# Optimization experiments

Measured on AMD Instinct MI355X. Metric: run time of the kernel, lower is better.

The kernel has to match this reference:

```python
import jax, jax.numpy as jnp
import numpy as np

N_NODES = 50000
N_EDGES = 800000
IN_CH = 16
OUT_CH = 16
HID = 32


def setup_inputs() -> dict:
    key = jax.random.key(0)
    ks = jax.random.split(key, 10)
    features = jax.random.normal(ks[0], (N_NODES, IN_CH), dtype=jnp.float32)
    coords = jax.random.normal(ks[1], (N_NODES, 3), dtype=jnp.float32)
    # edges without self-loops (avoids zero-distance edges)
    row = jax.random.randint(ks[2], (N_EDGES,), 0, N_NODES, dtype=jnp.int32)
    off = jax.random.randint(ks[3], (N_EDGES,), 1, N_NODES, dtype=jnp.int32)
    col = (row + off) % N_NODES
    edge_index = jnp.stack([row, col], axis=0)
    # params (fan-in scaled like torch defaults, roughly)
    w1 = jax.random.normal(ks[4], (1, HID), dtype=jnp.float32)
    b1 = jnp.zeros((HID,), dtype=jnp.float32)
    w2 = jax.random.normal(ks[5], (HID, HID), dtype=jnp.float32) / np.sqrt(HID)
    b2 = jnp.zeros((HID,), dtype=jnp.float32)
    wc = jax.random.normal(ks[6], (HID, IN_CH * OUT_CH), dtype=jnp.float32) / np.sqrt(HID)
    bc = jnp.zeros((IN_CH * OUT_CH,), dtype=jnp.float32)
    return {"features": features, "coords": coords, "edge_index": edge_index,
            "w1": w1, "b1": b1, "w2": w2, "b2": b2, "wc": wc, "bc": bc}


def reference(features, coords, edge_index, w1, b1, w2, b2, wc, bc):
    row, col = edge_index[0], edge_index[1]
    rel_pos = coords[row] - coords[col]                      # [E, 3]
    distances = jnp.sqrt(jnp.sum(rel_pos * rel_pos, axis=-1, keepdims=True))  # [E, 1]
    h = jax.nn.silu(distances @ w1 + b1)                     # [E, H]
    h = jax.nn.silu(h @ w2 + b2)                             # [E, H]
    coeffs = (h @ wc + bc).reshape(-1, OUT_CH, IN_CH)        # [E, out, in]
    # Faithful to torch einsum 'noi,ei->no': the edge axes of coeffs and
    # neighbor_features are DISTINCT labels, so features[col] is summed over
    # all edges, then contracted with each edge's coeff matrix.
    feat_sum = jnp.sum(features[col], axis=0)                # [in]
    messages = jnp.einsum('eoi,i->eo', coeffs, feat_sum)     # [E, out]
    out = jnp.zeros((features.shape[0], OUT_CH), dtype=features.dtype)
    out = out.at[row].add(messages)                          # scatter-add
    return out
```

## Files before the change

### kernel.cpp

```cpp
#include <hip/hip_runtime.h>
#include <hip/hip_bf16.h>

#define IN_CH 16
#define OUT_CH 16
#define HID 32
#define NSLICE 4
#define SDEG 32
#define CPAD 16
#define G_TAB 8192
#define DMAX 16.0f
#define RED_BLOCKS 64
#define TB 256

__device__ __forceinline__ float silu(float x) {
  return x * __frcp_rn(1.f + __expf(-x));
}

__global__ __launch_bounds__(256) void k_zero(int4* __restrict__ p, int n4) {
  int i = blockIdx.x * blockDim.x + threadIdx.x;
  if (i < n4) p[i] = make_int4(0, 0, 0, 0);
}

__global__ __launch_bounds__(256) void k_pass1(
    const float* __restrict__ feat, const float* __restrict__ coords,
    const int* __restrict__ row, const int* __restrict__ col, int E, int N,
    int* __restrict__ cnt_pad, float* __restrict__ bucket,
    float* __restrict__ partials) {
  int e = blockIdx.x * blockDim.x + threadIdx.x;
  int lane = threadIdx.x & 63;
  int wave = threadIdx.x >> 6;
  bool act = (e < E);

  float s[IN_CH];
#pragma unroll
  for (int i = 0; i < IN_CH; ++i) s[i] = 0.f;

  int r = 0, pos = SDEG;
  float d = 0.f;
  int slice = blockIdx.x & (NSLICE - 1);

  if (act) {
    r = row[e];
    int c = col[e];

    float rx = coords[r * 3 + 0] - coords[c * 3 + 0];
    float ry = coords[r * 3 + 1] - coords[c * 3 + 1];
    float rz = coords[r * 3 + 2] - coords[c * 3 + 2];
    d = sqrtf(rx * rx + ry * ry + rz * rz);

    pos = atomicAdd(&cnt_pad[((size_t)r * NSLICE + slice) * CPAD], 1);

    const float4* fp = reinterpret_cast<const float4*>(feat + (size_t)c * IN_CH);
    float4 a = fp[0], b = fp[1], cc = fp[2], dd = fp[3];
    s[0] = a.x;  s[1] = a.y;  s[2] = a.z;  s[3] = a.w;
    s[4] = b.x;  s[5] = b.y;  s[6] = b.z;  s[7] = b.w;
    s[8] = cc.x; s[9] = cc.y; s[10] = cc.z; s[11] = cc.w;
    s[12] = dd.x; s[13] = dd.y; s[14] = dd.z; s[15] = dd.w;
  }

  __shared__ float red[4][IN_CH];
#pragma unroll
  for (int i = 0; i < IN_CH; ++i) {
    float v = s[i];
#pragma unroll
    for (int off = 32; off > 0; off >>= 1) v += __shfl_down(v, off);
    s[i] = v;
  }
  if (lane == 0) {
#pragma unroll
    for (int i = 0; i < IN_CH; ++i) red[wave][i] = s[i];
  }
  __syncthreads();
  if (threadIdx.x < IN_CH) {
    int i = threadIdx.x;
    partials[(size_t)blockIdx.x * IN_CH + i] =
        red[0][i] + red[1][i] + red[2][i] + red[3][i];
  }

  if (act && pos < SDEG)
    bucket[((size_t)r * NSLICE + slice) * SDEG + pos] = d;
}

__global__ __launch_bounds__(256) void k_red(
    const float* __restrict__ partials, int nrows,
    const float* __restrict__ wc, const float* __restrict__ bc,
    float* __restrict__ stage2, int* __restrict__ done,
    float* __restrict__ wce, float* __restrict__ bce) {
  __shared__ float red[16][IN_CH];
  __shared__ float sfs[IN_CH];
  __shared__ int lastFlag;
  int t = threadIdx.x;
  int ch = t & 15, g = t >> 4;

  {
    int stream_id = blockIdx.x * 16 + g;
    int stride = 16 * RED_BLOCKS;
    float a = 0.f;
    for (int rr = stream_id; rr < nrows; rr += stride)
      a += partials[(size_t)rr * IN_CH + ch];
    red[g][ch] = a;
  }
  __syncthreads();
  if (t < IN_CH) {
    float s = 0.f;
#pragma unroll
    for (int g2 = 0; g2 < 16; ++g2) s += red[g2][t];
    stage2[blockIdx.x * IN_CH + t] = s;
  }
  __threadfence();
  __syncthreads();
  if (t == 0) lastFlag = (atomicAdd(done, 1) == RED_BLOCKS - 1);
  __syncthreads();
  if (!lastFlag) return;

  __threadfence();
  {
    int sg = t >> 4;
    float a = 0.f;
    for (int rr = sg; rr < RED_BLOCKS; rr += 16)
      a += stage2[rr * IN_CH + ch];
    red[sg][ch] = a;
  }
  __syncthreads();
  if (t < IN_CH) {
    float s = 0.f;
#pragma unroll
    for (int g2 = 0; g2 < 16; ++g2) s += red[g2][t];
    sfs[t] = s;
  }
  __syncthreads();

  for (int idx = t; idx < HID * OUT_CH; idx += 256) {
    int k = idx >> 4, o = idx & 15;
    float acc = 0.f;
#pragma unroll
    for (int i = 0; i < IN_CH; ++i)
      acc += wc[k * (IN_CH * OUT_CH) + o * IN_CH + i] * sfs[i];
    wce[idx] = acc;
  }
  if (t < OUT_CH) {
    float a = 0.f;
#pragma unroll
    for (int i = 0; i < IN_CH; ++i) a += bc[t * IN_CH + i] * sfs[i];
    bce[t] = a;
  }
}

__global__ __launch_bounds__(TB) void k_table(
    const float* __restrict__ w1, const float* __restrict__ b1,
    const float* __restrict__ w2, const float* __restrict__ b2,
    const float* __restrict__ wce, const float* __restrict__ bce,
    float* __restrict__ tableP) {
  __shared__ float F[TB][OUT_CH];
  int base = blockIdx.x * (TB - 1);
  int i = base + threadIdx.x;

  float m[OUT_CH];
#pragma unroll
  for (int o = 0; o < OUT_CH; ++o) m[o] = 0.f;

  if (i < G_TAB) {
    float d = (float)i * (DMAX / (float)(G_TAB - 1));

    float h1[HID];
#pragma unroll
    for (int k = 0; k < HID; ++k) h1[k] = silu(d * w1[k] + b1[k]);

    float h2[HID];
#pragma unroll
    for (int k = 0; k < HID; ++k) h2[k] = b2[k];
#pragma unroll
    for (int k = 0; k < HID; ++k) {
      float hk = h1[k];
#pragma unroll
      for (int j = 0; j < HID; ++j) h2[j] += hk * w2[k * HID + j];
    }

#pragma unroll
    for (int o = 0; o < OUT_CH; ++o) m[o] = bce[o];
#pragma unroll
    for (int k = 0; k < HID; ++k) {
      float hk = silu(h2[k]);
#pragma unroll
      for (int o = 0; o < OUT_CH; ++o) m[o] += hk * wce[k * OUT_CH + o];
    }
  }

#pragma unroll
  for (int o = 0; o < OUT_CH; ++o) F[threadIdx.x][o] = m[o];
  __syncthreads();

  const int NV4 = (TB - 1) * OUT_CH * 2 / 4;
  for (int v = threadIdx.x; v < NV4; v += TB) {
    int flat = v * 4;
    int p = flat >> 5;
    int w = flat & 31;
    int c0 = w >> 1;
    int P = base + p;
    if (P < G_TAB - 1) {
      float4 val = make_float4(F[p][c0], F[p + 1][c0],
                               F[p][c0 + 1], F[p + 1][c0 + 1]);
      *reinterpret_cast<float4*>(tableP + ((size_t)P * OUT_CH + c0) * 2) = val;
    }
  }
}

__global__ __launch_bounds__(256) void k_gather_tab(
    const int* __restrict__ cnt_pad, const float* __restrict__ bucket, int N,
    const float* __restrict__ tableP, float* __restrict__ out) {
  int wave = threadIdx.x >> 6;
  int lane = threadIdx.x & 63;
  int n = blockIdx.x * 4 + wave;
  if (n >= N) return;

  int g = lane >> 4;
  int ch = lane & 15;

  const float2* bp =
      reinterpret_cast<const float2*>(bucket + (size_t)n * (NSLICE * SDEG));
  float2 d2 = bp[lane];

  int c = 0;
  if (lane < NSLICE) c = cnt_pad[((size_t)n * NSLICE + lane) * CPAD];
  int c0 = min(__shfl(c, 0), SDEG);
  int c1 = min(__shfl(c, 1), SDEG);
  int c2 = min(__shfl(c, 2), SDEG);
  int c3 = min(__shfl(c, 3), SDEG);
  int cntG = (g == 0) ? c0 : (g == 1) ? c1 : (g == 2) ? c2 : c3;
  int jmax = max(max(c0, c1), max(c2, c3));

  const float inv = (float)(G_TAB - 1) / DMAX;
  float acc = 0.f;
  for (int j = 0; j < jmax; j += 2) {
    int half = (g * SDEG + j) >> 1;
    float da = __shfl(d2.x, half);
    float db = __shfl(d2.y, half);
    bool pa = (j < cntG), pb = (j + 1 < cntG);

    da = fminf(fmaxf(da, 0.f), DMAX);
    db = fminf(fmaxf(db, 0.f), DMAX);
    float xa = da * inv;
    int ia = min((int)xa, G_TAB - 2);
    float fa = xa - (float)ia;
    float xb = db * inv;
    int ib = min((int)xb, G_TAB - 2);
    float fb = xb - (float)ib;

    if (pa) {
      float2 F = *reinterpret_cast<const float2*>(
          tableP + ((size_t)ia * OUT_CH + ch) * 2);
      acc += F.x + fa * (F.y - F.x);
    }
    if (pb) {
      float2 F = *reinterpret_cast<const float2*>(
          tableP + ((size_t)ib * OUT_CH + ch) * 2);
      acc += F.x + fb * (F.y - F.x);
    }
  }

  acc += __shfl_xor(acc, 16);
  acc += __shfl_xor(acc, 32);
  if (lane < OUT_CH) out[(size_t)n * OUT_CH + lane] = acc;
}

__global__ __launch_bounds__(512) void k_wce_fb(
    const float* __restrict__ rows_in, int nrows,
    const float* __restrict__ wc, const float* __restrict__ bc,
    float* __restrict__ wce, float* __restrict__ bce) {
  __shared__ float seg[32][IN_CH];
  __shared__ float sfs[IN_CH];
  int t = threadIdx.x;
  {
    int ch = t & 15, sg = t >> 4;
    float a = 0.f;
    for (int rr = sg; rr < nrows; rr += 32)
      a += rows_in[(size_t)rr * IN_CH + ch];
    seg[sg][ch] = a;
  }
  __syncthreads();
  if (t < IN_CH) {
    float a = 0.f;
#pragma unroll
    for (int sg = 0; sg < 32; ++sg) a += seg[sg][t];
    sfs[t] = a;
  }
  __syncthreads();
  int k = t >> 4, o = t & 15;
  float acc = 0.f;
#pragma unroll
  for (int i = 0; i < IN_CH; ++i)
    acc += wc[k * (IN_CH * OUT_CH) + o * IN_CH + i] * sfs[i];
  wce[t] = acc;
  if (t < OUT_CH) {
    float a = 0.f;
#pragma unroll
    for (int i = 0; i < IN_CH; ++i) a += bc[t * IN_CH + i] * sfs[i];
    bce[t] = a;
  }
}

__global__ __launch_bounds__(256) void k_hist(
    const int* __restrict__ col, int E, int* __restrict__ ccnt) {
  int e = blockIdx.x * blockDim.x + threadIdx.x;
  if (e < E) atomicAdd(&ccnt[col[e]], 1);
}

__global__ __launch_bounds__(256) void k_fs(
    const float* __restrict__ feat, const int* __restrict__ ccnt, int N,
    float* __restrict__ partials) {
  int ch = threadIdx.x & 15;
  int slot = threadIdx.x >> 4;
  int gs = blockIdx.x * 16 + slot;
  int stride = 16 * gridDim.x;
  float a = 0.f;
  for (int n = gs; n < N; n += stride)
    a += (float)ccnt[n] * feat[(size_t)n * IN_CH + ch];
  __shared__ float red[16][IN_CH];
  red[slot][ch] = a;
  __syncthreads();
  if (threadIdx.x < IN_CH) {
    int i = threadIdx.x;
    float s = 0.f;
#pragma unroll
    for (int g = 0; g < 16; ++g) s += red[g][i];
    partials[(size_t)blockIdx.x * IN_CH + i] = s;
  }
}

__global__ __launch_bounds__(256) void k_edges_atomic(
    const float* __restrict__ coords, const int* __restrict__ row,
    const int* __restrict__ col, int E,
    const float* __restrict__ w1, const float* __restrict__ b1,
    const float* __restrict__ w2, const float* __restrict__ b2,
    const float* __restrict__ wce, const float* __restrict__ bce,
    float* __restrict__ out) {
  int e = blockIdx.x * blockDim.x + threadIdx.x;
  if (e >= E) return;
  int r = row[e], c = col[e];
  float rx = coords[r * 3 + 0] - coords[c * 3 + 0];
  float ry = coords[r * 3 + 1] - coords[c * 3 + 1];
  float rz = coords[r * 3 + 2] - coords[c * 3 + 2];
  float d = sqrtf(rx * rx + ry * ry + rz * rz);
  float h1[HID];
#pragma unroll
  for (int k = 0; k < HID; ++k) h1[k] = silu(d * w1[k] + b1[k]);
  float h2[HID];
#pragma unroll
  for (int k = 0; k < HID; ++k) h2[k] = b2[k];
#pragma unroll
  for (int k = 0; k < HID; ++k) {
    float hk = h1[k];
#pragma unroll
    for (int j = 0; j < HID; ++j) h2[j] += hk * w2[k * HID + j];
  }
  float m[OUT_CH];
#pragma unroll
  for (int o = 0; o < OUT_CH; ++o) m[o] = bce[o];
#pragma unroll
  for (int k = 0; k < HID; ++k) {
    float hk = silu(h2[k]);
#pragma unroll
    for (int o = 0; o < OUT_CH; ++o) m[o] += hk * wce[k * OUT_CH + o];
  }
  float* op = out + (size_t)r * OUT_CH;
#pragma unroll
  for (int o = 0; o < OUT_CH; ++o) atomicAdd(op + o, m[o]);
}

extern "C" void kernel_launch(void* const* d_in, const int* in_sizes, int n_in,
                              void* d_out, int out_size, void* d_ws,
                              size_t ws_size, hipStream_t stream) {
  const float* features = (const float*)d_in[0];
  const float* coords   = (const float*)d_in[1];
  const int*   eidx     = (const int*)d_in[2];
  const float* w1       = (const float*)d_in[3];
  const float* b1       = (const float*)d_in[4];
  const float* w2       = (const float*)d_in[5];
  const float* b2       = (const float*)d_in[6];
  const float* wc       = (const float*)d_in[7];
  const float* bc       = (const float*)d_in[8];

  const int E = in_sizes[2] / 2;
  const int N = in_sizes[0] / IN_CH;
  const int* row = eidx;
  const int* col = eidx + E;

  float* out = (float*)d_out;
  float* ws  = (float*)d_ws;
  const int eb = (E + 255) / 256;

  size_t off = 0;
  float* wce = ws + off;      off += 512;
  float* bce = ws + off;      off += 16;
  float* stage2 = ws + off;   off += RED_BLOCKS * IN_CH;
  float* partials = ws + off; off += (size_t)eb * IN_CH;
  off = (off + 63) & ~(size_t)63;
  float* tableP = ws + off;   off += (size_t)G_TAB * OUT_CH * 2;
  off = (off + 63) & ~(size_t)63;
  int* done = (int*)(ws + off);     off += 16;
  int* cnt_pad = (int*)(ws + off);  off += (size_t)N * NSLICE * CPAD;
  float* bucket = ws + off;         off += (size_t)N * NSLICE * SDEG;
  size_t needed = off * 4;

  if (ws_size >= needed) {
    int n4 = (int)((16 + (size_t)N * NSLICE * CPAD) / 4);
    k_zero<<<(n4 + 255) / 256, 256, 0, stream>>>((int4*)done, n4);
    k_pass1<<<eb, 256, 0, stream>>>(features, coords, row, col, E, N, cnt_pad,
                                    bucket, partials);
    k_red<<<RED_BLOCKS, 256, 0, stream>>>(partials, eb, wc, bc, stage2, done,
                                          wce, bce);
    int tb_grid = (G_TAB - 1 + (TB - 1) - 1) / (TB - 1) + 1;
    k_table<<<tb_grid, TB, 0, stream>>>(w1, b1, w2, b2, wce, bce, tableP);
    int gb = (N + 3) / 4;
    k_gather_tab<<<gb, 256, 0, stream>>>(cnt_pad, bucket, N, tableP, out);
  } else {
    float* partials_fb = bce + 16;
    int*   ccnt_fb     = (int*)(partials_fb + 64 * IN_CH);
    int nz4 = (N + 3) / 4;
    k_zero<<<(nz4 + 255) / 256, 256, 0, stream>>>((int4*)ccnt_fb, nz4);
    hipMemsetAsync(out, 0, (size_t)out_size * sizeof(float), stream);
    k_hist<<<(E + 255) / 256, 256, 0, stream>>>(col, E, ccnt_fb);
    k_fs<<<64, 256, 0, stream>>>(features, ccnt_fb, N, partials_fb);
    k_wce_fb<<<1, 512, 0, stream>>>(partials_fb, 64, wc, bc, wce, bce);
    k_edges_atomic<<<(E + 255) / 256, 256, 0, stream>>>(coords, row, col, E,
                                                        w1, b1, w2, b2, wce,
                                                        bce, out);
  }
}
```

Baseline: 101.1 us.

## Compact slice counters, interleave bucket layout, make gather persistent with prefetch

Per-node slice counters are no longer padded to 16 ints each. They are packed into four contiguous ints, which shrinks the buffer that has to be zeroed every call and makes the count reads dense. The distance bucket is reordered to [node][pos][slice], so one 64-lane load covers the first 16 positions of all slices; positions beyond 16 are read from global memory. The gather kernel becomes a grid-stride persistent kernel of 1024 blocks that prefetches the next node's bucket and counts. The distance clamp to DMAX is dropped in favour of clamping only the table index, so distances above DMAX would extrapolate past the last table entry.

```diff
diff --git a/kernel.cpp b/kernel.cpp
--- a/kernel.cpp
+++ b/kernel.cpp
@@ -6,11 +6,11 @@
 #define HID 32
 #define NSLICE 4
 #define SDEG 32
-#define CPAD 16
 #define G_TAB 8192
 #define DMAX 16.0f
 #define RED_BLOCKS 64
 #define TB 256
+#define GB_BLOCKS 1024
 
 __device__ __forceinline__ float silu(float x) {
   return x * __frcp_rn(1.f + __expf(-x));
@@ -24,7 +24,7 @@
 __global__ __launch_bounds__(256) void k_pass1(
     const float* __restrict__ feat, const float* __restrict__ coords,
     const int* __restrict__ row, const int* __restrict__ col, int E, int N,
-    int* __restrict__ cnt_pad, float* __restrict__ bucket,
+    int* __restrict__ cnt4, float* __restrict__ bucket,
     float* __restrict__ partials) {
   int e = blockIdx.x * blockDim.x + threadIdx.x;
   int lane = threadIdx.x & 63;
@@ -48,7 +48,7 @@
     float rz = coords[r * 3 + 2] - coords[c * 3 + 2];
     d = sqrtf(rx * rx + ry * ry + rz * rz);
 
-    pos = atomicAdd(&cnt_pad[((size_t)r * NSLICE + slice) * CPAD], 1);
+    pos = atomicAdd(&cnt4[r * NSLICE + slice], 1);
 
     const float4* fp = reinterpret_cast<const float4*>(feat + (size_t)c * IN_CH);
     float4 a = fp[0], b = fp[1], cc = fp[2], dd = fp[3];
@@ -78,7 +78,7 @@
   }
 
   if (act && pos < SDEG)
-    bucket[((size_t)r * NSLICE + slice) * SDEG + pos] = d;
+    bucket[((size_t)r * SDEG + pos) * NSLICE + slice] = d;
 }
 
 __global__ __launch_bounds__(256) void k_red(
@@ -206,61 +206,75 @@
 }
 
 __global__ __launch_bounds__(256) void k_gather_tab(
-    const int* __restrict__ cnt_pad, const float* __restrict__ bucket, int N,
+    const int* __restrict__ cnt4, const float* __restrict__ bucket, int N,
     const float* __restrict__ tableP, float* __restrict__ out) {
   int wave = threadIdx.x >> 6;
   int lane = threadIdx.x & 63;
+  int g = lane >> 4;
+  int ch = lane & 15;
+  const int nwaves = GB_BLOCKS * 4;
+
   int n = blockIdx.x * 4 + wave;
   if (n >= N) return;
 
-  int g = lane >> 4;
-  int ch = lane & 15;
-
-  const float2* bp =
-      reinterpret_cast<const float2*>(bucket + (size_t)n * (NSLICE * SDEG));
-  float2 d2 = bp[lane];
-
-  int c = 0;
-  if (lane < NSLICE) c = cnt_pad[((size_t)n * NSLICE + lane) * CPAD];
-  int c0 = min(__shfl(c, 0), SDEG);
-  int c1 = min(__shfl(c, 1), SDEG);
-  int c2 = min(__shfl(c, 2), SDEG);
-  int c3 = min(__shfl(c, 3), SDEG);
-  int cntG = (g == 0) ? c0 : (g == 1) ? c1 : (g == 2) ? c2 : c3;
-  int jmax = max(max(c0, c1), max(c2, c3));
-
   const float inv = (float)(G_TAB - 1) / DMAX;
-  float acc = 0.f;
-  for (int j = 0; j < jmax; j += 2) {
-    int half = (g * SDEG + j) >> 1;
-    float da = __shfl(d2.x, half);
-    float db = __shfl(d2.y, half);
-    bool pa = (j < cntG), pb = (j + 1 < cntG);
-
-    da = fminf(fmaxf(da, 0.f), DMAX);
-    db = fminf(fmaxf(db, 0.f), DMAX);
-    float xa = da * inv;
-    int ia = min((int)xa, G_TAB - 2);
-    float fa = xa - (float)ia;
-    float xb = db * inv;
-    int ib = min((int)xb, G_TAB - 2);
-    float fb = xb - (float)ib;
-
-    if (pa) {
-      float2 F = *reinterpret_cast<const float2*>(
-          tableP + ((size_t)ia * OUT_CH + ch) * 2);
-      acc += F.x + fa * (F.y - F.x);
+
+  float dpre = bucket[(size_t)n * (SDEG * NSLICE) + lane];
+  int cpre = (lane < NSLICE) ? cnt4[n * NSLICE + lane] : 0;
+
+  while (true) {
+    float dcur = dpre;
+    int ccur = cpre;
+    int nn = n + nwaves;
+    if (nn < N) {
+      dpre = bucket[(size_t)nn * (SDEG * NSLICE) + lane];
+      cpre = (lane < NSLICE) ? cnt4[nn * NSLICE + lane] : 0;
     }
-    if (pb) {
-      float2 F = *reinterpret_cast<const float2*>(
-          tableP + ((size_t)ib * OUT_CH + ch) * 2);
-      acc += F.x + fb * (F.y - F.x);
+
+    int c0 = min(__shfl(ccur, 0), SDEG);
+    int c1 = min(__shfl(ccur, 1), SDEG);
+    int c2 = min(__shfl(ccur, 2), SDEG);
+    int c3 = min(__shfl(ccur, 3), SDEG);
+    int cntG = (g == 0) ? c0 : (g == 1) ? c1 : (g == 2) ? c2 : c3;
+    int jmax = max(max(c0, c1), max(c2, c3));
+
+    const float* nb = bucket + (size_t)n * (SDEG * NSLICE);
+    float acc = 0.f;
+    for (int j = 0; j < jmax; j += 2) {
+      float da = __shfl(dcur, j * NSLICE + g);
+      float db = __shfl(dcur, (j + 1) * NSLICE + g);
+      if (j >= 16) da = nb[j * NSLICE + g];
+      if (j + 1 >= 16) db = nb[(j + 1) * NSLICE + g];
+      bool pa = (j < cntG), pb = (j + 1 < cntG);
+
+      float xa = da * inv;
+      int ia = (int)xa;
+      ia = ia < 0 ? 0 : (ia > G_TAB - 2 ? G_TAB - 2 : ia);
+      float fa = xa - (float)ia;
+      float xb = db * inv;
+      int ib = (int)xb;
+      ib = ib < 0 ? 0 : (ib > G_TAB - 2 ? G_TAB - 2 : ib);
+      float fb = xb - (float)ib;
+
+      if (pa) {
+        float2 F = *reinterpret_cast<const float2*>(
+            tableP + ((size_t)ia * OUT_CH + ch) * 2);
+        acc += F.x + fa * (F.y - F.x);
+      }
+      if (pb) {
+        float2 F = *reinterpret_cast<const float2*>(
+            tableP + ((size_t)ib * OUT_CH + ch) * 2);
+        acc += F.x + fb * (F.y - F.x);
+      }
     }
-  }
-
-  acc += __shfl_xor(acc, 16);
-  acc += __shfl_xor(acc, 32);
-  if (lane < OUT_CH) out[(size_t)n * OUT_CH + lane] = acc;
+
+    acc += __shfl_xor(acc, 16);
+    acc += __shfl_xor(acc, 32);
+    if (lane < OUT_CH) out[(size_t)n * OUT_CH + lane] = acc;
+
+    if (nn >= N) break;
+    n = nn;
+  }
 }
 
 __global__ __launch_bounds__(512) void k_wce_fb(
@@ -397,22 +411,23 @@
   off = (off + 63) & ~(size_t)63;
   float* tableP = ws + off;   off += (size_t)G_TAB * OUT_CH * 2;
   off = (off + 63) & ~(size_t)63;
-  int* done = (int*)(ws + off);     off += 16;
-  int* cnt_pad = (int*)(ws + off);  off += (size_t)N * NSLICE * CPAD;
-  float* bucket = ws + off;         off += (size_t)N * NSLICE * SDEG;
+  int* done = (int*)(ws + off);   off += 16;
+  int* cnt4 = (int*)(ws + off);   off += (size_t)N * NSLICE;
+  off = (off + 63) & ~(size_t)63;
+  float* bucket = ws + off;       off += (size_t)N * NSLICE * SDEG;
   size_t needed = off * 4;
 
   if (ws_size >= needed) {
-    int n4 = (int)((16 + (size_t)N * NSLICE * CPAD) / 4);
+    int n4 = (int)((16 + (size_t)N * NSLICE) / 4);
     k_zero<<<(n4 + 255) / 256, 256, 0, stream>>>((int4*)done, n4);
-    k_pass1<<<eb, 256, 0, stream>>>(features, coords, row, col, E, N, cnt_pad,
+    k_pass1<<<eb, 256, 0, stream>>>(features, coords, row, col, E, N, cnt4,
                                     bucket, partials);
     k_red<<<RED_BLOCKS, 256, 0, stream>>>(partials, eb, wc, bc, stage2, done,
                                           wce, bce);
     int tb_grid = (G_TAB - 1 + (TB - 1) - 1) / (TB - 1) + 1;
     k_table<<<tb_grid, TB, 0, stream>>>(w1, b1, w2, b2, wce, bce, tableP);
-    int gb = (N + 3) / 4;
-    k_gather_tab<<<gb, 256, 0, stream>>>(cnt_pad, bucket, N, tableP, out);
+    int gb = min(GB_BLOCKS, (N + 3) / 4);
+    k_gather_tab<<<gb, 256, 0, stream>>>(cnt4, bucket, N, tableP, out);
   } else {
     float* partials_fb = bce + 16;
     int*   ccnt_fb     = (int*)(partials_fb + 64 * IN_CH);
```

Result: slower. 110.6 us (+9.5%).
